# Kernel tuning notes

Hardware: AMD Instinct MI355X
Metric: run time of the kernel (lower is better)

The kernel has to match this reference:

```python
import jax, jax.numpy as jnp
import numpy as np

B, N, F = 2, 512, 128
NUM_BASIS = 4


def _mlp(x, W1, b1, W2, b2, W3, b3):
    # two hidden ReLU layers, linear output -> [..., NUM_BASIS]
    h = jax.nn.relu(x @ W1 + b1)
    h = jax.nn.relu(h @ W2 + b2)
    return h @ W3 + b3


def setup_inputs() -> dict:
    key = jax.random.key(0)
    ks = jax.random.split(key, 12)
    s = 0.05  # keep activations O(1)
    inp = {
        "pointwise_features": jax.random.normal(ks[0], (B, N, F), jnp.float32),
        "relative_features": jax.random.normal(ks[1], (B, N, N, F), jnp.float32),
        "pointwise_basis": jax.random.normal(ks[2], (B, N, NUM_BASIS, 3), jnp.float32),
        "relative_basis": jax.random.normal(ks[3], (B, N, N, NUM_BASIS, 3), jnp.float32),
        "pw_W1": jax.random.normal(ks[4], (F, 128), jnp.float32) * s,
        "pw_b1": jnp.zeros((128,), jnp.float32),
        "pw_W2": jax.random.normal(ks[5], (128, 128), jnp.float32) * s,
        "pw_b2": jnp.zeros((128,), jnp.float32),
        "pw_W3": jax.random.normal(ks[6], (128, NUM_BASIS), jnp.float32) * s,
        "pw_b3": jnp.zeros((NUM_BASIS,), jnp.float32),
        "rel_W1": jax.random.normal(ks[7], (F, 128), jnp.float32) * s,
        "rel_b1": jnp.zeros((128,), jnp.float32),
        "rel_W2": jax.random.normal(ks[8], (128, 128), jnp.float32) * s,
        "rel_b2": jnp.zeros((128,), jnp.float32),
        "rel_W3": jax.random.normal(ks[9], (128, NUM_BASIS), jnp.float32) * s,
        "rel_b3": jnp.zeros((NUM_BASIS,), jnp.float32),
        # last 64 atoms are padding (masked) in every batch element
        "masked_elements": jnp.broadcast_to(jnp.arange(N) >= N - 64, (B, N)),
    }
    return inp


def reference(pointwise_features, relative_features, pointwise_basis, relative_basis,
              pw_W1, pw_b1, pw_W2, pw_b2, pw_W3, pw_b3,
              rel_W1, rel_b1, rel_W2, rel_b2, rel_W3, rel_b3,
              masked_elements):
    unmasked = ~masked_elements                      # [B, N]
    num_atoms = unmasked.sum(-1).astype(pointwise_features.dtype)  # [B]

    # pointwise_shift: [B, N, K, 3]
    pw_scale = _mlp(pointwise_features, pw_W1, pw_b1, pw_W2, pw_b2, pw_W3, pw_b3)
    pointwise_shift = pointwise_basis * pw_scale[..., None]

    # relative_shift: [B, N, N, K, 3], mask over j, mean over j
    rel_scale = _mlp(relative_features, rel_W1, rel_b1, rel_W2, rel_b2, rel_W3, rel_b3)
    relative_shift = relative_basis * rel_scale[..., None]
    relative_shift = relative_shift * unmasked[:, None, :, None, None]
    relative_shift = relative_shift.sum(-3) / num_atoms[:, None, None, None]  # [B, N, K, 3]

    all_shifts = pointwise_shift + relative_shift
    shift = all_shifts.sum(-2) / num_atoms[:, None, None]  # [B, N, 3]
    return shift
```

## Files before the change

kernel.cpp:

```cpp
#include <hip/hip_runtime.h>
#include <stdint.h>

#define LDK 136

typedef __attribute__((ext_vector_type(4))) float f32x4;
typedef __attribute__((ext_vector_type(8))) short bf16x8;

__device__ inline unsigned short f2bf_rtne(float f) {
    union { float f; unsigned u; } v; v.f = f;
    unsigned u = v.u;
    u += 0x7fffu + ((u >> 16) & 1u);
    return (unsigned short)(u >> 16);
}
__device__ inline float bf2f(unsigned short h) {
    union { float f; unsigned u; } v; v.u = ((unsigned)h) << 16;
    return v.f;
}

__global__ void prep_kernel(const float* __restrict__ relW1, const float* __restrict__ relW2,
                            const float* __restrict__ pwW1, const float* __restrict__ pwW2,
                            const void* __restrict__ maskp,
                            float* __restrict__ maskf, float* __restrict__ na,
                            unsigned short* __restrict__ w1T_rel, unsigned short* __restrict__ w2T_rel,
                            unsigned short* __restrict__ w1T_pw, unsigned short* __restrict__ w2T_pw) {
    int t = threadIdx.x;
    const float* srcs[4] = {relW1, relW2, pwW1, pwW2};
    unsigned short* dsts[4] = {w1T_rel, w2T_rel, w1T_pw, w2T_pw};
    int e0 = blockIdx.x * 1024 + t;
#pragma unroll
    for (int i = 0; i < 4; ++i) {
        int e = e0 + i * 256;
        int mat = e >> 14, o = e & 16383;
        int n = o >> 7, k = o & 127;
        dsts[mat][o] = f2bf_rtne(srcs[mat][k * 128 + n]);
    }
    if (blockIdx.x == 0) {
        __shared__ int anyb;
        __shared__ float cnt[2];
        if (t == 0) anyb = 0;
        if (t < 2) cnt[t] = 0.f;
        __syncthreads();
        const unsigned char* mb = (const unsigned char*)maskp;
        int la = 0;
        for (int i = t; i < 1024; i += 256) la |= mb[i];
        if (la) atomicOr(&anyb, 1);
        __syncthreads();
        bool isbyte = (anyb != 0);
        const int* mi = (const int*)maskp;
        float loc0 = 0.f, loc1 = 0.f;
        for (int i = t; i < 1024; i += 256) {
            int v = isbyte ? (int)mb[i] : mi[i];
            float um = (v != 0) ? 0.f : 1.f;
            maskf[i] = um;
            if (i < 512) loc0 += um; else loc1 += um;
        }
        atomicAdd(&cnt[0], loc0);
        atomicAdd(&cnt[1], loc1);
        __syncthreads();
        if (t < 2) na[t] = cnt[t];
    }
}

__global__ __launch_bounds__(256, 2)
void mlp_kernel(const float* __restrict__ X,
                const unsigned short* __restrict__ w1T,
                const unsigned short* __restrict__ w2T,
                const float* __restrict__ W3, const float* __restrict__ b1,
                const float* __restrict__ b2, const float* __restrict__ b3,
                float* __restrict__ Sout) {
    __shared__ short xs[2][64 * LDK];
    __shared__ short hs[64 * LDK];
    __shared__ float w3s[4 * 128];
    __shared__ float bs1[128], bs2[128], b3s[4];

    int t = threadIdx.x;
    int w = t >> 6, lane = t & 63, q = lane >> 4, col = lane & 15;

    if (t < 128) { bs1[t] = b1[t]; bs2[t] = b2[t]; }
    if (t < 4) b3s[t] = b3[t];
    for (int i = t; i < 512; i += 256) { int c = i >> 2, k = i & 3; w3s[k * 128 + c] = W3[i]; }

    bf16x8 w1f[2][4], w2f[2][4];
#pragma unroll
    for (int tn = 0; tn < 2; ++tn)
#pragma unroll
        for (int kc = 0; kc < 4; ++kc) {
            int n = w * 32 + tn * 16 + col;
            int kk = kc * 32 + q * 8;
            w1f[tn][kc] = *(const bf16x8*)&w1T[n * 128 + kk];
            w2f[tn][kc] = *(const bf16x8*)&w2T[n * 128 + kk];
        }

    long rowbase = (long)blockIdx.x * 256;
    int r0 = t >> 5, cg = t & 31;

    float4 px[8];
    {
        const float4* Xg = (const float4*)(X + rowbase * 128);
#pragma unroll
        for (int i = 0; i < 8; ++i) px[i] = Xg[(r0 + 8 * i) * 32 + cg];
#pragma unroll
        for (int i = 0; i < 8; ++i) {
            float4 v = px[i];
            short4 s4 = make_short4((short)f2bf_rtne(v.x), (short)f2bf_rtne(v.y),
                                    (short)f2bf_rtne(v.z), (short)f2bf_rtne(v.w));
            *(short4*)&xs[0][(r0 + 8 * i) * LDK + cg * 4] = s4;
        }
    }
    __syncthreads();

    for (int tile = 0; tile < 4; ++tile) {
        int buf = tile & 1;
        if (tile < 3) {
            const float4* Xg2 = (const float4*)(X + (rowbase + (long)(tile + 1) * 64) * 128);
#pragma unroll
            for (int i = 0; i < 8; ++i) px[i] = Xg2[(r0 + 8 * i) * 32 + cg];
        }

        f32x4 acc[2][4];
#pragma unroll
        for (int tn = 0; tn < 2; ++tn)
#pragma unroll
            for (int tm = 0; tm < 4; ++tm) acc[tn][tm] = (f32x4)(0.f);
#pragma unroll
        for (int kc = 0; kc < 4; ++kc) {
            bf16x8 bf[4];
#pragma unroll
            for (int tm = 0; tm < 4; ++tm)
                bf[tm] = *(const bf16x8*)&xs[buf][(tm * 16 + col) * LDK + kc * 32 + q * 8];
#pragma unroll
            for (int tn = 0; tn < 2; ++tn)
#pragma unroll
                for (int tm = 0; tm < 4; ++tm)
                    acc[tn][tm] = __builtin_amdgcn_mfma_f32_16x16x32_bf16(w1f[tn][kc], bf[tm], acc[tn][tm], 0, 0, 0);
        }
        __syncthreads();

#pragma unroll
        for (int tn = 0; tn < 2; ++tn)
#pragma unroll
            for (int tm = 0; tm < 4; ++tm) {
                int n0 = w * 32 + tn * 16 + q * 4;
                int m = tm * 16 + col;
                float4 bb = *(const float4*)&bs1[n0];
                short4 s4 = make_short4(
                    (short)f2bf_rtne(fmaxf(acc[tn][tm][0] + bb.x, 0.f)),
                    (short)f2bf_rtne(fmaxf(acc[tn][tm][1] + bb.y, 0.f)),
                    (short)f2bf_rtne(fmaxf(acc[tn][tm][2] + bb.z, 0.f)),
                    (short)f2bf_rtne(fmaxf(acc[tn][tm][3] + bb.w, 0.f)));
                *(short4*)&hs[m * LDK + n0] = s4;
            }
        if (tile < 3) {
#pragma unroll
            for (int i = 0; i < 8; ++i) {
                float4 v = px[i];
                short4 s4 = make_short4((short)f2bf_rtne(v.x), (short)f2bf_rtne(v.y),
                                        (short)f2bf_rtne(v.z), (short)f2bf_rtne(v.w));
                *(short4*)&xs[1 - buf][(r0 + 8 * i) * LDK + cg * 4] = s4;
            }
        }
        __syncthreads();

        f32x4 acc2[2][4];
#pragma unroll
        for (int tn = 0; tn < 2; ++tn)
#pragma unroll
            for (int tm = 0; tm < 4; ++tm) acc2[tn][tm] = (f32x4)(0.f);
#pragma unroll
        for (int kc = 0; kc < 4; ++kc) {
            bf16x8 bf[4];
#pragma unroll
            for (int tm = 0; tm < 4; ++tm)
                bf[tm] = *(const bf16x8*)&hs[(tm * 16 + col) * LDK + kc * 32 + q * 8];
#pragma unroll
            for (int tn = 0; tn < 2; ++tn)
#pragma unroll
                for (int tm = 0; tm < 4; ++tm)
                    acc2[tn][tm] = __builtin_amdgcn_mfma_f32_16x16x32_bf16(w2f[tn][kc], bf[tm], acc2[tn][tm], 0, 0, 0);
        }
        __syncthreads();

#pragma unroll
        for (int tn = 0; tn < 2; ++tn)
#pragma unroll
            for (int tm = 0; tm < 4; ++tm) {
                int n0 = w * 32 + tn * 16 + q * 4;
                int m = tm * 16 + col;
                float4 bb = *(const float4*)&bs2[n0];
                short4 s4 = make_short4(
                    (short)f2bf_rtne(fmaxf(acc2[tn][tm][0] + bb.x, 0.f)),
                    (short)f2bf_rtne(fmaxf(acc2[tn][tm][1] + bb.y, 0.f)),
                    (short)f2bf_rtne(fmaxf(acc2[tn][tm][2] + bb.z, 0.f)),
                    (short)f2bf_rtne(fmaxf(acc2[tn][tm][3] + bb.w, 0.f)));
                *(short4*)&hs[m * LDK + n0] = s4;
            }
        __syncthreads();

        {
            int row = t >> 2, k = t & 3;
            float s = b3s[k];
#pragma unroll
            for (int cc = 0; cc < 16; ++cc) {
                bf16x8 h8 = *(const bf16x8*)&hs[row * LDK + cc * 8];
                float4 wa = *(const float4*)&w3s[k * 128 + cc * 8];
                float4 wb = *(const float4*)&w3s[k * 128 + cc * 8 + 4];
                s += bf2f((unsigned short)h8[0]) * wa.x + bf2f((unsigned short)h8[1]) * wa.y +
                     bf2f((unsigned short)h8[2]) * wa.z + bf2f((unsigned short)h8[3]) * wa.w +
                     bf2f((unsigned short)h8[4]) * wb.x + bf2f((unsigned short)h8[5]) * wb.y +
                     bf2f((unsigned short)h8[6]) * wb.z + bf2f((unsigned short)h8[7]) * wb.w;
            }
            Sout[(rowbase + (long)tile * 64) * 4 + t] = s;
        }
    }
}

__global__ __launch_bounds__(256)
void reduce_kernel(const float* __restrict__ S_rel, const float* __restrict__ S_pw,
                   const float* __restrict__ rel_basis, const float* __restrict__ pw_basis,
                   const float* __restrict__ maskf, const float* __restrict__ na,
                   float* __restrict__ out) {
    int bi = blockIdx.x;
    int b = bi >> 9;
    int t = threadIdx.x;
    float part[12];
#pragma unroll
    for (int r = 0; r < 12; ++r) part[r] = 0.f;

    for (int j = t; j < 512; j += 256) {
        float m = maskf[b * 512 + j];
        long r = (long)bi * 512 + j;
        float4 s4 = *(const float4*)&S_rel[r * 4];
        const float* bp = &rel_basis[r * 12];
        float4 q0 = *(const float4*)&bp[0];
        float4 q1 = *(const float4*)&bp[4];
        float4 q2 = *(const float4*)&bp[8];
        float s0 = s4.x * m, s1 = s4.y * m, s2 = s4.z * m, s3 = s4.w * m;
        part[0] += s0 * q0.x; part[1] += s0 * q0.y; part[2]  += s0 * q0.z;
        part[3] += s1 * q0.w; part[4] += s1 * q1.x; part[5]  += s1 * q1.y;
        part[6] += s2 * q1.z; part[7] += s2 * q1.w; part[8]  += s2 * q2.x;
        part[9] += s3 * q2.y; part[10] += s3 * q2.z; part[11] += s3 * q2.w;
    }

    __shared__ float red[256][12];
#pragma unroll
    for (int r = 0; r < 12; ++r) red[t][r] = part[r];
    __syncthreads();
    for (int s = 128; s > 0; s >>= 1) {
        if (t < s) {
#pragma unroll
            for (int r = 0; r < 12; ++r) red[t][r] += red[t + s][r];
        }
        __syncthreads();
    }
    if (t < 3) {
        float NA = na[b];
        float accp = 0.f, rel = 0.f;
#pragma unroll
        for (int k = 0; k < 4; ++k) {
            accp += pw_basis[bi * 12 + k * 3 + t] * S_pw[bi * 4 + k];
            rel  += red[0][k * 3 + t];
        }
        out[bi * 3 + t] = accp / NA + rel / (NA * NA);
    }
}

extern "C" void kernel_launch(void* const* d_in, const int* in_sizes, int n_in,
                              void* d_out, int out_size, void* d_ws, size_t ws_size,
                              hipStream_t stream) {
    const float* pw_feat   = (const float*)d_in[0];
    const float* rel_feat  = (const float*)d_in[1];
    const float* pw_basis  = (const float*)d_in[2];
    const float* rel_basis = (const float*)d_in[3];
    const float* pw_W1 = (const float*)d_in[4];
    const float* pw_b1 = (const float*)d_in[5];
    const float* pw_W2 = (const float*)d_in[6];
    const float* pw_b2 = (const float*)d_in[7];
    const float* pw_W3 = (const float*)d_in[8];
    const float* pw_b3 = (const float*)d_in[9];
    const float* rel_W1 = (const float*)d_in[10];
    const float* rel_b1 = (const float*)d_in[11];
    const float* rel_W2 = (const float*)d_in[12];
    const float* rel_b2 = (const float*)d_in[13];
    const float* rel_W3 = (const float*)d_in[14];
    const float* rel_b3 = (const float*)d_in[15];
    const void*  maskp  = d_in[16];
    float* out = (float*)d_out;

    char* ws = (char*)d_ws;
    float* maskf = (float*)(ws + 0);
    float* na    = (float*)(ws + 4096);
    unsigned short* w1T_rel = (unsigned short*)(ws + 4352);
    unsigned short* w2T_rel = (unsigned short*)(ws + 4352 + 32768);
    unsigned short* w1T_pw  = (unsigned short*)(ws + 4352 + 65536);
    unsigned short* w2T_pw  = (unsigned short*)(ws + 4352 + 98304);
    float* S_pw  = (float*)(ws + 4352 + 131072);
    float* S_rel = (float*)(ws + 4352 + 131072 + 16384);

    prep_kernel<<<64, 256, 0, stream>>>(rel_W1, rel_W2, pw_W1, pw_W2, maskp,
                                        maskf, na, w1T_rel, w2T_rel, w1T_pw, w2T_pw);
    mlp_kernel<<<2048, 256, 0, stream>>>(rel_feat, w1T_rel, w2T_rel, rel_W3,
                                         rel_b1, rel_b2, rel_b3, S_rel);
    mlp_kernel<<<4, 256, 0, stream>>>(pw_feat, w1T_pw, w2T_pw, pw_W3,
                                      pw_b1, pw_b2, pw_b3, S_pw);
    reduce_kernel<<<1024, 256, 0, stream>>>(S_rel, S_pw, rel_basis, pw_basis,
                                            maskf, na, out);
}
```

Baseline: 462.1 us.

## Compute MLP output layer with MFMA, restructure LDS buffers, use shuffle reduction

```diff
diff --git a/kernel.cpp b/kernel.cpp
--- a/kernel.cpp
+++ b/kernel.cpp
@@ -12,17 +12,15 @@
     u += 0x7fffu + ((u >> 16) & 1u);
     return (unsigned short)(u >> 16);
 }
-__device__ inline float bf2f(unsigned short h) {
-    union { float f; unsigned u; } v; v.u = ((unsigned)h) << 16;
-    return v.f;
-}
 
 __global__ void prep_kernel(const float* __restrict__ relW1, const float* __restrict__ relW2,
                             const float* __restrict__ pwW1, const float* __restrict__ pwW2,
+                            const float* __restrict__ relW3, const float* __restrict__ pwW3,
                             const void* __restrict__ maskp,
                             float* __restrict__ maskf, float* __restrict__ na,
                             unsigned short* __restrict__ w1T_rel, unsigned short* __restrict__ w2T_rel,
-                            unsigned short* __restrict__ w1T_pw, unsigned short* __restrict__ w2T_pw) {
+                            unsigned short* __restrict__ w1T_pw, unsigned short* __restrict__ w2T_pw,
+                            unsigned short* __restrict__ w3T_rel, unsigned short* __restrict__ w3T_pw) {
     int t = threadIdx.x;
     const float* srcs[4] = {relW1, relW2, pwW1, pwW2};
     unsigned short* dsts[4] = {w1T_rel, w2T_rel, w1T_pw, w2T_pw};
@@ -33,6 +31,13 @@
         int mat = e >> 14, o = e & 16383;
         int n = o >> 7, k = o & 127;
         dsts[mat][o] = f2bf_rtne(srcs[mat][k * 128 + n]);
+    }
+    if (blockIdx.x == 1) {
+        for (int i = t; i < 2048; i += 256) {
+            int r = i >> 7, h = i & 127;
+            w3T_rel[i] = (r < 4) ? f2bf_rtne(relW3[h * 4 + r]) : (unsigned short)0;
+            w3T_pw[i]  = (r < 4) ? f2bf_rtne(pwW3[h * 4 + r])  : (unsigned short)0;
+        }
     }
     if (blockIdx.x == 0) {
         __shared__ int anyb;
@@ -65,12 +70,12 @@
 void mlp_kernel(const float* __restrict__ X,
                 const unsigned short* __restrict__ w1T,
                 const unsigned short* __restrict__ w2T,
-                const float* __restrict__ W3, const float* __restrict__ b1,
-                const float* __restrict__ b2, const float* __restrict__ b3,
+                const unsigned short* __restrict__ w3T,
+                const float* __restrict__ b1, const float* __restrict__ b2,
+                const float* __restrict__ b3,
                 float* __restrict__ Sout) {
-    __shared__ short xs[2][64 * LDK];
-    __shared__ short hs[64 * LDK];
-    __shared__ float w3s[4 * 128];
+    __shared__ short xs[64 * LDK];
+    __shared__ short hs[2][64 * LDK];
     __shared__ float bs1[128], bs2[128], b3s[4];
 
     int t = threadIdx.x;
@@ -78,9 +83,8 @@
 
     if (t < 128) { bs1[t] = b1[t]; bs2[t] = b2[t]; }
     if (t < 4) b3s[t] = b3[t];
-    for (int i = t; i < 512; i += 256) { int c = i >> 2, k = i & 3; w3s[k * 128 + c] = W3[i]; }
-
-    bf16x8 w1f[2][4], w2f[2][4];
+
+    bf16x8 w1f[2][4], w2f[2][4], w3f[4];
 #pragma unroll
     for (int tn = 0; tn < 2; ++tn)
 #pragma unroll
@@ -90,6 +94,9 @@
             w1f[tn][kc] = *(const bf16x8*)&w1T[n * 128 + kk];
             w2f[tn][kc] = *(const bf16x8*)&w2T[n * 128 + kk];
         }
+#pragma unroll
+    for (int kc = 0; kc < 4; ++kc)
+        w3f[kc] = *(const bf16x8*)&w3T[col * 128 + kc * 32 + q * 8];
 
     long rowbase = (long)blockIdx.x * 256;
     int r0 = t >> 5, cg = t & 31;
@@ -104,13 +111,13 @@
             float4 v = px[i];
             short4 s4 = make_short4((short)f2bf_rtne(v.x), (short)f2bf_rtne(v.y),
                                     (short)f2bf_rtne(v.z), (short)f2bf_rtne(v.w));
-            *(short4*)&xs[0][(r0 + 8 * i) * LDK + cg * 4] = s4;
+            *(short4*)&xs[(r0 + 8 * i) * LDK + cg * 4] = s4;
         }
     }
     __syncthreads();
 
     for (int tile = 0; tile < 4; ++tile) {
-        int buf = tile & 1;
+        int hp = tile & 1;
         if (tile < 3) {
             const float4* Xg2 = (const float4*)(X + (rowbase + (long)(tile + 1) * 64) * 128);
 #pragma unroll
@@ -127,14 +134,13 @@
             bf16x8 bf[4];
 #pragma unroll
             for (int tm = 0; tm < 4; ++tm)
-                bf[tm] = *(const bf16x8*)&xs[buf][(tm * 16 + col) * LDK + kc * 32 + q * 8];
+                bf[tm] = *(const bf16x8*)&xs[(tm * 16 + col) * LDK + kc * 32 + q * 8];
 #pragma unroll
             for (int tn = 0; tn < 2; ++tn)
 #pragma unroll
                 for (int tm = 0; tm < 4; ++tm)
                     acc[tn][tm] = __builtin_amdgcn_mfma_f32_16x16x32_bf16(w1f[tn][kc], bf[tm], acc[tn][tm], 0, 0, 0);
         }
-        __syncthreads();
 
 #pragma unroll
         for (int tn = 0; tn < 2; ++tn)
@@ -148,18 +154,19 @@
                     (short)f2bf_rtne(fmaxf(acc[tn][tm][1] + bb.y, 0.f)),
                     (short)f2bf_rtne(fmaxf(acc[tn][tm][2] + bb.z, 0.f)),
                     (short)f2bf_rtne(fmaxf(acc[tn][tm][3] + bb.w, 0.f)));
-                *(short4*)&hs[m * LDK + n0] = s4;
-            }
+                *(short4*)&hs[hp][m * LDK + n0] = s4;
+            }
+        __syncthreads();
+
         if (tile < 3) {
 #pragma unroll
             for (int i = 0; i < 8; ++i) {
                 float4 v = px[i];
                 short4 s4 = make_short4((short)f2bf_rtne(v.x), (short)f2bf_rtne(v.y),
                                         (short)f2bf_rtne(v.z), (short)f2bf_rtne(v.w));
-                *(short4*)&xs[1 - buf][(r0 + 8 * i) * LDK + cg * 4] = s4;
-            }
-        }
-        __syncthreads();
+                *(short4*)&xs[(r0 + 8 * i) * LDK + cg * 4] = s4;
+            }
+        }
 
         f32x4 acc2[2][4];
 #pragma unroll
@@ -171,7 +178,7 @@
             bf16x8 bf[4];
 #pragma unroll
             for (int tm = 0; tm < 4; ++tm)
-                bf[tm] = *(const bf16x8*)&hs[(tm * 16 + col) * LDK + kc * 32 + q * 8];
+                bf[tm] = *(const bf16x8*)&hs[hp][(tm * 16 + col) * LDK + kc * 32 + q * 8];
 #pragma unroll
             for (int tn = 0; tn < 2; ++tn)
 #pragma unroll
@@ -192,24 +199,22 @@
                     (short)f2bf_rtne(fmaxf(acc2[tn][tm][1] + bb.y, 0.f)),
                     (short)f2bf_rtne(fmaxf(acc2[tn][tm][2] + bb.z, 0.f)),
                     (short)f2bf_rtne(fmaxf(acc2[tn][tm][3] + bb.w, 0.f)));
-                *(short4*)&hs[m * LDK + n0] = s4;
+                *(short4*)&hs[hp][m * LDK + n0] = s4;
             }
         __syncthreads();
 
         {
-            int row = t >> 2, k = t & 3;
-            float s = b3s[k];
-#pragma unroll
-            for (int cc = 0; cc < 16; ++cc) {
-                bf16x8 h8 = *(const bf16x8*)&hs[row * LDK + cc * 8];
-                float4 wa = *(const float4*)&w3s[k * 128 + cc * 8];
-                float4 wb = *(const float4*)&w3s[k * 128 + cc * 8 + 4];
-                s += bf2f((unsigned short)h8[0]) * wa.x + bf2f((unsigned short)h8[1]) * wa.y +
-                     bf2f((unsigned short)h8[2]) * wa.z + bf2f((unsigned short)h8[3]) * wa.w +
-                     bf2f((unsigned short)h8[4]) * wb.x + bf2f((unsigned short)h8[5]) * wb.y +
-                     bf2f((unsigned short)h8[6]) * wb.z + bf2f((unsigned short)h8[7]) * wb.w;
-            }
-            Sout[(rowbase + (long)tile * 64) * 4 + t] = s;
+            f32x4 a3 = (f32x4)(0.f);
+#pragma unroll
+            for (int kc = 0; kc < 4; ++kc) {
+                bf16x8 hb = *(const bf16x8*)&hs[hp][(w * 16 + col) * LDK + kc * 32 + q * 8];
+                a3 = __builtin_amdgcn_mfma_f32_16x16x32_bf16(w3f[kc], hb, a3, 0, 0, 0);
+            }
+            if (q == 0) {
+                long r = rowbase + (long)tile * 64 + w * 16 + col;
+                *(float4*)&Sout[r * 4] = make_float4(a3[0] + b3s[0], a3[1] + b3s[1],
+                                                     a3[2] + b3s[2], a3[3] + b3s[3]);
+            }
         }
     }
 }
@@ -241,24 +246,25 @@
         part[9] += s3 * q2.y; part[10] += s3 * q2.z; part[11] += s3 * q2.w;
     }
 
-    __shared__ float red[256][12];
-#pragma unroll
-    for (int r = 0; r < 12; ++r) red[t][r] = part[r];
+#pragma unroll
+    for (int s = 32; s > 0; s >>= 1)
+#pragma unroll
+        for (int r = 0; r < 12; ++r) part[r] += __shfl_down(part[r], s);
+
+    __shared__ float red[4][12];
+    int w = t >> 6, lane = t & 63;
+    if (lane == 0)
+#pragma unroll
+        for (int r = 0; r < 12; ++r) red[w][r] = part[r];
     __syncthreads();
-    for (int s = 128; s > 0; s >>= 1) {
-        if (t < s) {
-#pragma unroll
-            for (int r = 0; r < 12; ++r) red[t][r] += red[t + s][r];
-        }
-        __syncthreads();
-    }
+
     if (t < 3) {
         float NA = na[b];
         float accp = 0.f, rel = 0.f;
 #pragma unroll
         for (int k = 0; k < 4; ++k) {
+            rel  += red[0][k * 3 + t] + red[1][k * 3 + t] + red[2][k * 3 + t] + red[3][k * 3 + t];
             accp += pw_basis[bi * 12 + k * 3 + t] * S_pw[bi * 4 + k];
-            rel  += red[0][k * 3 + t];
         }
         out[bi * 3 + t] = accp / NA + rel / (NA * NA);
     }
@@ -290,17 +296,20 @@
     float* maskf = (float*)(ws + 0);
     float* na    = (float*)(ws + 4096);
     unsigned short* w1T_rel = (unsigned short*)(ws + 4352);
-    unsigned short* w2T_rel = (unsigned short*)(ws + 4352 + 32768);
-    unsigned short* w1T_pw  = (unsigned short*)(ws + 4352 + 65536);
-    unsigned short* w2T_pw  = (unsigned short*)(ws + 4352 + 98304);
-    float* S_pw  = (float*)(ws + 4352 + 131072);
-    float* S_rel = (float*)(ws + 4352 + 131072 + 16384);
-
-    prep_kernel<<<64, 256, 0, stream>>>(rel_W1, rel_W2, pw_W1, pw_W2, maskp,
-                                        maskf, na, w1T_rel, w2T_rel, w1T_pw, w2T_pw);
-    mlp_kernel<<<2048, 256, 0, stream>>>(rel_feat, w1T_rel, w2T_rel, rel_W3,
+    unsigned short* w2T_rel = (unsigned short*)(ws + 37120);
+    unsigned short* w1T_pw  = (unsigned short*)(ws + 69888);
+    unsigned short* w2T_pw  = (unsigned short*)(ws + 102656);
+    unsigned short* w3T_rel = (unsigned short*)(ws + 135424);
+    unsigned short* w3T_pw  = (unsigned short*)(ws + 139520);
+    float* S_pw  = (float*)(ws + 143616);
+    float* S_rel = (float*)(ws + 160000);
+
+    prep_kernel<<<64, 256, 0, stream>>>(rel_W1, rel_W2, pw_W1, pw_W2, rel_W3, pw_W3, maskp,
+                                        maskf, na, w1T_rel, w2T_rel, w1T_pw, w2T_pw,
+                                        w3T_rel, w3T_pw);
+    mlp_kernel<<<2048, 256, 0, stream>>>(rel_feat, w1T_rel, w2T_rel, w3T_rel,
                                          rel_b1, rel_b2, rel_b3, S_rel);
-    mlp_kernel<<<4, 256, 0, stream>>>(pw_feat, w1T_pw, w2T_pw, pw_W3,
+    mlp_kernel<<<4, 256, 0, stream>>>(pw_feat, w1T_pw, w2T_pw, w3T_pw,
                                       pw_b1, pw_b2, pw_b3, S_pw);
     reduce_kernel<<<1024, 256, 0, stream>>>(S_rel, S_pw, rel_basis, pw_basis,
                                             maskf, na, out);
```

Measured after the change: 446.0 us. 1.04x faster.
